# Optimization experiments

Measured on AMD Instinct MI355X. Metric: run time of the kernel, lower is better.

Reference implementation:

```python
import jax, jax.numpy as jnp
import numpy as np

N_NODES = 50000
N_EDGES = 800000
IN_C, HID_C, OUT_C = 128, 128, 64


def setup_inputs() -> dict:
    key = jax.random.key(0)
    k1, k2, k3, k4, k5 = jax.random.split(key, 5)
    x = jax.random.normal(k1, (N_NODES, IN_C), dtype=jnp.float32)
    edge_index = jax.random.randint(k2, (2, N_EDGES), 0, N_NODES, dtype=jnp.int64)
    # Glorot-style init for GCN weights, zero bias (PyG GCNConv defaults)
    s1 = (6.0 / (IN_C + HID_C)) ** 0.5
    s2 = (6.0 / (HID_C + OUT_C)) ** 0.5
    W1 = jax.random.uniform(k3, (IN_C, HID_C), jnp.float32, -s1, s1)
    W2 = jax.random.uniform(k4, (HID_C, OUT_C), jnp.float32, -s2, s2)
    b1 = jnp.zeros((HID_C,), jnp.float32)
    b2 = jnp.zeros((OUT_C,), jnp.float32)
    return {"x": x, "edge_index": edge_index, "W1": W1, "b1": b1, "W2": W2, "b2": b2}


def _gcn_conv(x, src, dst, W, b, n_nodes):
    # PyG GCNConv: add self-loops, symmetric normalization, linear transform,
    # scatter-add aggregation from src (row) to dst (col), then bias.
    h = x @ W  # [N, out]
    loops = jnp.arange(n_nodes, dtype=src.dtype)
    src_f = jnp.concatenate([src, loops])
    dst_f = jnp.concatenate([dst, loops])
    deg = jax.ops.segment_sum(jnp.ones_like(dst_f, dtype=h.dtype), dst_f,
                              num_segments=n_nodes)  # in-degree incl. self-loop
    dinv = jnp.where(deg > 0, jax.lax.rsqrt(deg), 0.0)
    norm = dinv[src_f] * dinv[dst_f]  # [E + N]
    msgs = h[src_f] * norm[:, None]   # gather + scale
    out = jax.ops.segment_sum(msgs, dst_f, num_segments=n_nodes)  # scatter-add
    return out + b


def reference(x, edge_index, W1, b1, W2, b2):
    src, dst = edge_index[0], edge_index[1]
    n = x.shape[0]
    h = jax.nn.relu(_gcn_conv(x, src, dst, W1, b1, n))
    return _gcn_conv(h, src, dst, W2, b2, n)
```

## Files before the change

kernel.cpp:

```cpp
#include <hip/hip_runtime.h>
#include <hip/hip_bf16.h>
#include <hip/hip_fp16.h>


#define NBUCK 800
#define CHUNK 2048
#define STASH 2048

typedef float f32x4 __attribute__((ext_vector_type(4)));
typedef _Float16 f16x8 __attribute__((ext_vector_type(8)));

__global__ __launch_bounds__(256) void presort_k(const int* __restrict__ src,
                                                 const int* __restrict__ dst,
                                                 unsigned* __restrict__ rec2,
                                                 int* __restrict__ hist2,
                                                 int* __restrict__ runstart2,
                                                 int E) {
    __shared__ int lh[NBUCK], lscan[NBUCK], cur[NBUCK];
    __shared__ int sred[256];
    __shared__ unsigned srec[CHUNK];
    int t = threadIdx.x;
    int lo = blockIdx.x * CHUNK, hi = min(E, lo + CHUNK);

    for (int i = t; i < NBUCK; i += 256) lh[i] = 0;
    __syncthreads();
    for (int e = lo + t; e < hi; e += 256)
        atomicAdd(&lh[dst[e] >> 6], 1);
    __syncthreads();

    int base = t * 4;
    int v[4];
    int s = 0;
#pragma unroll
    for (int i = 0; i < 4; ++i) {
        int idx = base + i;
        int c = (idx < NBUCK) ? lh[idx] : 0;
        v[i] = c; s += c;
    }
    sred[t] = s;
    __syncthreads();
#pragma unroll
    for (int off = 1; off < 256; off <<= 1) {
        int x = 0;
        if (t >= off) x = sred[t - off];
        __syncthreads();
        sred[t] += x;
        __syncthreads();
    }
    int run = sred[t] - s;
#pragma unroll
    for (int i = 0; i < 4; ++i) {
        int idx = base + i;
        if (idx < NBUCK) { lscan[idx] = run; cur[idx] = run; }
        run += v[i];
    }
    __syncthreads();

    for (int e = lo + t; e < hi; e += 256) {
        int d = dst[e];
        int p = atomicAdd(&cur[d >> 6], 1);
        srec[p] = (unsigned)(src[e] & 0xffff) | ((unsigned)d << 16);
    }
    __syncthreads();

    int n = hi - lo;
    for (int j = t; j < n; j += 256) rec2[lo + j] = srec[j];
    int hbase = blockIdx.x * NBUCK;
    for (int b = t; b < NBUCK; b += 256) {
        hist2[hbase + b] = lh[b];
        runstart2[hbase + b] = lscan[b];
    }
}

__global__ __launch_bounds__(256) void coltot_k(const int* __restrict__ hist2,
                                                int* __restrict__ btot, int BCNT) {
    __shared__ int sred[256];
    int b = blockIdx.x, t = threadIdx.x;
    int s = 0;
    for (int i = t; i < BCNT; i += 256) s += hist2[i * NBUCK + b];
    sred[t] = s;
    __syncthreads();
#pragma unroll
    for (int off = 128; off > 0; off >>= 1) {
        if (t < off) sred[t] += sred[t + off];
        __syncthreads();
    }
    if (t == 0) btot[b] = sred[0];
}

__global__ __launch_bounds__(256) void scan800_k(const int* __restrict__ btot,
                                                 int* __restrict__ bucketBase,
                                                 int* __restrict__ offsets,
                                                 int N, int E) {
    __shared__ int sred[256];
    int t = threadIdx.x;
    int base = t * 4;
    int v[4];
    int s = 0;
#pragma unroll
    for (int i = 0; i < 4; ++i) {
        int idx = base + i;
        int c = (idx < NBUCK) ? btot[idx] : 0;
        v[i] = c; s += c;
    }
    sred[t] = s;
    __syncthreads();
#pragma unroll
    for (int off = 1; off < 256; off <<= 1) {
        int x = 0;
        if (t >= off) x = sred[t - off];
        __syncthreads();
        sred[t] += x;
        __syncthreads();
    }
    int run = sred[t] - s;
#pragma unroll
    for (int i = 0; i < 4; ++i) {
        int idx = base + i;
        if (idx < NBUCK) bucketBase[idx] = run;
        run += v[i];
    }
    if (t == 255) bucketBase[NBUCK] = run;
    if (t == 0) offsets[N] = E;
}

__global__ __launch_bounds__(256) void finish2_k(const unsigned* __restrict__ rec2,
                                                 const int* __restrict__ hist2,
                                                 const int* __restrict__ runstart2,
                                                 const int* __restrict__ bucketBase,
                                                 int* __restrict__ offsets,
                                                 float* __restrict__ dinv,
                                                 unsigned short* __restrict__ adj,
                                                 int BCNT, int N) {
    __shared__ int ncnt[64], ncur[64], nodeOff[64];
    __shared__ int stashCnt;
    __shared__ unsigned stash[STASH];
    __shared__ unsigned short adjl[STASH];
    int b = blockIdx.x, t = threadIdx.x;
    if (t < 64) { ncnt[t] = 0; ncur[t] = 0; }
    if (t == 0) stashCnt = 0;
    __syncthreads();

    for (int i = t; i < BCNT; i += 256) {
        int len = hist2[i * NBUCK + b];
        if (!len) continue;
        int gbase = i * CHUNK + runstart2[i * NBUCK + b];
        int sp = atomicAdd(&stashCnt, len);
        for (int k = 0; k < len; ++k) {
            unsigned r = rec2[gbase + k];
            atomicAdd(&ncnt[(r >> 16) & 63], 1);
            if (sp + k < STASH) stash[sp + k] = r;
        }
    }
    __syncthreads();

    if (t == 0) {
        int r = 0;
#pragma unroll
        for (int i = 0; i < 64; ++i) { nodeOff[i] = r; r += ncnt[i]; }
    }
    __syncthreads();

    int bstart = bucketBase[b];
    if (t < 64) {
        int gnode = b * 64 + t;
        if (gnode < N) {
            dinv[gnode] = rsqrtf((float)(ncnt[t] + 1));
            offsets[gnode] = bstart + nodeOff[t];
        }
    }
    __syncthreads();

    int tot = stashCnt;
    if (tot > STASH) tot = STASH;
    for (int j = t; j < tot; j += 256) {
        unsigned r = stash[j];
        int ln = (r >> 16) & 63;
        int p = atomicAdd(&ncur[ln], 1);
        adjl[nodeOff[ln] + p] = (unsigned short)(r & 0xffff);
    }
    __syncthreads();
    for (int j = t; j < tot; j += 256) adj[bstart + j] = adjl[j];
}

template <int NOUT, bool HALF_IN>
__global__ __launch_bounds__(256) void gemm_mfma_k(const void* __restrict__ Xv,
                                                   const float* __restrict__ W,
                                                   const float* __restrict__ dinv,
                                                   __half* __restrict__ Hout, int M) {
    constexpr int K = 128;
    constexpr int BM = 64;
    constexpr int LDP = K + 8;
    constexpr int CT = NOUT / 16;
    __shared__ _Float16 xs[BM][LDP];
    __shared__ _Float16 wsl[NOUT][LDP];

    int t = threadIdx.x;
    int brow = blockIdx.x * BM;

    if constexpr (HALF_IN) {
        const __half* X = (const __half*)Xv;
        for (int i = t; i < BM * (K / 8); i += 256) {
            int row = i / (K / 8), c8 = i % (K / 8);
            int gr = brow + row;
            union { _Float16 h[8]; uint4 u; } pk;
            if (gr < M) {
                uint4 u = *(const uint4*)(X + (size_t)gr * K + c8 * 8);
                const __half2* hp = (const __half2*)&u;
                float di = dinv[gr];
#pragma unroll
                for (int j = 0; j < 4; ++j) {
                    float2 f = __half22float2(hp[j]);
                    pk.h[2 * j] = (_Float16)(f.x * di);
                    pk.h[2 * j + 1] = (_Float16)(f.y * di);
                }
            } else {
                pk.u = make_uint4(0, 0, 0, 0);
            }
            *(uint4*)&xs[row][c8 * 8] = pk.u;
        }
    } else {
        const float* X = (const float*)Xv;
        for (int i = t; i < BM * (K / 4); i += 256) {
            int row = i / (K / 4), c4 = i % (K / 4);
            int gr = brow + row;
            union { _Float16 h[4]; uint2 u; } pk;
            if (gr < M) {
                float4 v = *(const float4*)(X + (size_t)gr * K + c4 * 4);
                float di = dinv[gr];
                pk.h[0] = (_Float16)(v.x * di);
                pk.h[1] = (_Float16)(v.y * di);
                pk.h[2] = (_Float16)(v.z * di);
                pk.h[3] = (_Float16)(v.w * di);
            } else {
                pk.u = make_uint2(0, 0);
            }
            *(uint2*)&xs[row][c4 * 4] = pk.u;
        }
    }

    for (int i = t; i < K * (NOUT / 4); i += 256) {
        int k = i / (NOUT / 4), c4 = i % (NOUT / 4);
        float4 wv = *(const float4*)(W + (size_t)k * NOUT + c4 * 4);
        wsl[c4 * 4 + 0][k] = (_Float16)wv.x;
        wsl[c4 * 4 + 1][k] = (_Float16)wv.y;
        wsl[c4 * 4 + 2][k] = (_Float16)wv.z;
        wsl[c4 * 4 + 3][k] = (_Float16)wv.w;
    }
    __syncthreads();

    int w = t >> 6, lane = t & 63;
    int lrow = lane & 15;
    int lko = (lane >> 4) * 8;

    f32x4 acc[CT];
#pragma unroll
    for (int c = 0; c < CT; ++c) acc[c] = (f32x4){0.f, 0.f, 0.f, 0.f};

#pragma unroll
    for (int s = 0; s < K / 32; ++s) {
        f16x8 a = *(const f16x8*)&xs[w * 16 + lrow][s * 32 + lko];
#pragma unroll
        for (int c = 0; c < CT; ++c) {
            f16x8 b = *(const f16x8*)&wsl[c * 16 + lrow][s * 32 + lko];
            acc[c] = __builtin_amdgcn_mfma_f32_16x16x32_f16(a, b, acc[c], 0, 0, 0);
        }
    }

    __syncthreads();
#pragma unroll
    for (int c = 0; c < CT; ++c) {
#pragma unroll
        for (int r = 0; r < 4; ++r)
            xs[w * 16 + (lane >> 4) * 4 + r][c * 16 + lrow] = (_Float16)acc[c][r];
    }
    __syncthreads();
    for (int j = t; j < BM * (NOUT / 8); j += 256) {
        int row = j / (NOUT / 8), c8 = j % (NOUT / 8);
        int gr = brow + row;
        if (gr < M)
            *(uint4*)(Hout + (size_t)gr * NOUT + c8 * 8) = *(uint4*)&xs[row][c8 * 8];
    }
}

__device__ __forceinline__ void ld_row(const __half* p, float (&f)[4]) {
    uint2 u = *(const uint2*)p;
    const __half2* hp = (const __half2*)&u;
    float2 a = __half22float2(hp[0]);
    float2 b = __half22float2(hp[1]);
    f[0] = a.x; f[1] = a.y; f[2] = b.x; f[3] = b.y;
}
__device__ __forceinline__ void ld_row(const __half* p, float (&f)[2]) {
    float2 a = __half22float2(*(const __half2*)p);
    f[0] = a.x; f[1] = a.y;
}

template <int C, bool RELU, typename TOUT>
__global__ __launch_bounds__(256) void aggregate_k(const __half* __restrict__ H,
                                                   const int* __restrict__ offsets,
                                                   const unsigned short* __restrict__ adj,
                                                   const float* __restrict__ dinv,
                                                   const float* __restrict__ bias,
                                                   TOUT* __restrict__ out, int n) {
    constexpr int V = C / 32;
    int wave = threadIdx.x >> 6;
    int lane = threadIdx.x & 63;
    int half_id = lane >> 5;
    int sub = lane & 31;
    int node = blockIdx.x * 8 + wave * 2 + half_id;
    if (node >= n) return;

    const __half* hl = H + sub * V;

    float acc[V];
    ld_row(hl + (size_t)node * C, acc);

    int e0 = offsets[node], e1 = offsets[node + 1];
    int e = e0;

    for (; e + 8 <= e1; e += 8) {
        int s[8];
#pragma unroll
        for (int j = 0; j < 8; ++j) s[j] = adj[e + j];
        float t[8][V];
#pragma unroll
        for (int j = 0; j < 8; ++j) ld_row(hl + (size_t)s[j] * C, t[j]);
#pragma unroll
        for (int v = 0; v < V; ++v)
            acc[v] += ((t[0][v] + t[1][v]) + (t[2][v] + t[3][v])) +
                      ((t[4][v] + t[5][v]) + (t[6][v] + t[7][v]));
    }
    for (; e + 2 <= e1; e += 2) {
        int s0 = adj[e], s1 = adj[e + 1];
        float t0[V], t1[V];
        ld_row(hl + (size_t)s0 * C, t0);
        ld_row(hl + (size_t)s1 * C, t1);
#pragma unroll
        for (int v = 0; v < V; ++v) acc[v] += t0[v] + t1[v];
    }
    if (e < e1) {
        float t0[V];
        ld_row(hl + (size_t)adj[e] * C, t0);
#pragma unroll
        for (int v = 0; v < V; ++v) acc[v] += t0[v];
    }

    float di = dinv[node];
    float o[V];
#pragma unroll
    for (int v = 0; v < V; ++v) {
        o[v] = acc[v] * di + bias[sub * V + v];
        if (RELU) o[v] = fmaxf(o[v], 0.f);
    }

    if constexpr (sizeof(TOUT) == 2) {
        union { __half2 h[2]; uint2 u; } pk;
        pk.h[0] = __floats2half2_rn(o[0], o[1]);
        pk.h[1] = __floats2half2_rn(o[2], o[3]);
        *(uint2*)((__half*)out + (size_t)node * C + sub * V) = pk.u;
    } else {
        *(float2*)((float*)out + (size_t)node * C + sub * V) = make_float2(o[0], o[1]);
    }
}

extern "C" void kernel_launch(void* const* d_in, const int* in_sizes, int n_in,
                              void* d_out, int out_size, void* d_ws, size_t ws_size,
                              hipStream_t stream) {
    const float* x = (const float*)d_in[0];
    const int* ei = (const int*)d_in[1];
    const float* W1 = (const float*)d_in[2];
    const float* b1 = (const float*)d_in[3];
    const float* W2 = (const float*)d_in[4];
    const float* b2 = (const float*)d_in[5];
    float* out = (float*)d_out;

    const int IN_C = 128, HID_C = 128;
    int N = in_sizes[0] / IN_C;
    int E = in_sizes[1] / 2;
    const int* src = ei;
    const int* dst = ei + E;

    int BCNT = (E + CHUNK - 1) / CHUNK;

    int NP = (N + 255) & ~255;
    int EP = (E + 255) & ~255;
    char* w = (char*)d_ws;
    int* hist2 = (int*)w;           w += (size_t)BCNT * NBUCK * 4;
    int* runstart2 = (int*)w;       w += (size_t)BCNT * NBUCK * 4;
    int* btot = (int*)w;            w += (size_t)(NBUCK + 32) * 4;
    int* bucketBase = (int*)w;      w += (size_t)(NBUCK + 32) * 4;
    int* offsets = (int*)w;         w += (size_t)(NP + 256) * 4;
    float* dinv = (float*)w;        w += (size_t)NP * 4;
    unsigned* rec2 = (unsigned*)w;  w += (size_t)(BCNT * CHUNK) * 4;
    unsigned short* adj = (unsigned short*)w; w += (size_t)EP * 2;
    __half* H1 = (__half*)w;        w += (size_t)NP * HID_C * 2;
    __half* HID = (__half*)w;       w += (size_t)NP * HID_C * 2;
    (void)ws_size; (void)n_in; (void)out_size;

    presort_k<<<BCNT, 256, 0, stream>>>(src, dst, rec2, hist2, runstart2, E);
    coltot_k<<<NBUCK, 256, 0, stream>>>(hist2, btot, BCNT);
    scan800_k<<<1, 256, 0, stream>>>(btot, bucketBase, offsets, N, E);
    finish2_k<<<NBUCK, 256, 0, stream>>>(rec2, hist2, runstart2, bucketBase,
                                         offsets, dinv, adj, BCNT, N);

    gemm_mfma_k<128, false><<<(N + 63) / 64, 256, 0, stream>>>(x, W1, dinv, H1, N);
    aggregate_k<128, true, __half><<<(N + 7) / 8, 256, 0, stream>>>(
        H1, offsets, adj, dinv, b1, HID, N);

    gemm_mfma_k<64, true><<<(N + 63) / 64, 256, 0, stream>>>(HID, W2, dinv, H1, N);
    aggregate_k<64, false, float><<<(N + 7) / 8, 256, 0, stream>>>(
        H1, offsets, adj, dinv, b2, out, N);
}
```

Before: 123.6 us.

## Split each node's edge list across four lane groups with wider row loads

The aggregation kernel now gives each node a full wave: four 16-lane groups each gather a quarter of the neighbor rows, and the partial sums are combined with cross-lane shuffles. Each lane loads 8 (or 4) halves per row instead of 4 (or 2), so row loads are wider, and the unrolled-by-8 loop with its tail loops is replaced by a single predicated 16-edge loop. The aim is more independent gathers in flight per node and lower latency on the average degree of about 16. In exchange, a quarter of the lanes sit idle on short or ragged edge lists, shuffle reductions are added, and the grid now covers 4 nodes per block instead of 8.

Result: slower. 145.0 us (+17.3%).

```diff
diff --git a/kernel.cpp b/kernel.cpp
--- a/kernel.cpp
+++ b/kernel.cpp
@@ -283,16 +283,21 @@
     }
 }
 
+__device__ __forceinline__ void ld_row(const __half* p, float (&f)[8]) {
+    uint4 u = *(const uint4*)p;
+    const __half2* hp = (const __half2*)&u;
+#pragma unroll
+    for (int j = 0; j < 4; ++j) {
+        float2 a = __half22float2(hp[j]);
+        f[2 * j] = a.x; f[2 * j + 1] = a.y;
+    }
+}
 __device__ __forceinline__ void ld_row(const __half* p, float (&f)[4]) {
     uint2 u = *(const uint2*)p;
     const __half2* hp = (const __half2*)&u;
     float2 a = __half22float2(hp[0]);
     float2 b = __half22float2(hp[1]);
     f[0] = a.x; f[1] = a.y; f[2] = b.x; f[3] = b.y;
-}
-__device__ __forceinline__ void ld_row(const __half* p, float (&f)[2]) {
-    float2 a = __half22float2(*(const __half2*)p);
-    f[0] = a.x; f[1] = a.y;
 }
 
 template <int C, bool RELU, typename TOUT>
@@ -302,64 +307,64 @@
                                                    const float* __restrict__ dinv,
                                                    const float* __restrict__ bias,
                                                    TOUT* __restrict__ out, int n) {
-    constexpr int V = C / 32;
+    constexpr int V = C / 16;
     int wave = threadIdx.x >> 6;
     int lane = threadIdx.x & 63;
-    int half_id = lane >> 5;
-    int sub = lane & 31;
-    int node = blockIdx.x * 8 + wave * 2 + half_id;
+    int q = lane >> 4;
+    int sub = lane & 15;
+    int node = blockIdx.x * 4 + wave;
     if (node >= n) return;
 
     const __half* hl = H + sub * V;
 
     float acc[V];
-    ld_row(hl + (size_t)node * C, acc);
+#pragma unroll
+    for (int v = 0; v < V; ++v) acc[v] = 0.f;
+    if (q == 0) ld_row(hl + (size_t)node * C, acc);
 
     int e0 = offsets[node], e1 = offsets[node + 1];
-    int e = e0;
-
-    for (; e + 8 <= e1; e += 8) {
-        int s[8];
-#pragma unroll
-        for (int j = 0; j < 8; ++j) s[j] = adj[e + j];
-        float t[8][V];
-#pragma unroll
-        for (int j = 0; j < 8; ++j) ld_row(hl + (size_t)s[j] * C, t[j]);
+
+    for (int eb = e0; eb < e1; eb += 16) {
+        float t[4][V];
+#pragma unroll
+        for (int j = 0; j < 4; ++j) {
+            int idx = eb + j * 4 + q;
+            if (idx < e1) {
+                ld_row(hl + (size_t)adj[idx] * C, t[j]);
+            } else {
+#pragma unroll
+                for (int v = 0; v < V; ++v) t[j][v] = 0.f;
+            }
+        }
 #pragma unroll
         for (int v = 0; v < V; ++v)
-            acc[v] += ((t[0][v] + t[1][v]) + (t[2][v] + t[3][v])) +
-                      ((t[4][v] + t[5][v]) + (t[6][v] + t[7][v]));
-    }
-    for (; e + 2 <= e1; e += 2) {
-        int s0 = adj[e], s1 = adj[e + 1];
-        float t0[V], t1[V];
-        ld_row(hl + (size_t)s0 * C, t0);
-        ld_row(hl + (size_t)s1 * C, t1);
-#pragma unroll
-        for (int v = 0; v < V; ++v) acc[v] += t0[v] + t1[v];
-    }
-    if (e < e1) {
-        float t0[V];
-        ld_row(hl + (size_t)adj[e] * C, t0);
-#pragma unroll
-        for (int v = 0; v < V; ++v) acc[v] += t0[v];
-    }
-
-    float di = dinv[node];
-    float o[V];
+            acc[v] += (t[0][v] + t[1][v]) + (t[2][v] + t[3][v]);
+    }
+
 #pragma unroll
     for (int v = 0; v < V; ++v) {
-        o[v] = acc[v] * di + bias[sub * V + v];
-        if (RELU) o[v] = fmaxf(o[v], 0.f);
-    }
-
-    if constexpr (sizeof(TOUT) == 2) {
-        union { __half2 h[2]; uint2 u; } pk;
-        pk.h[0] = __floats2half2_rn(o[0], o[1]);
-        pk.h[1] = __floats2half2_rn(o[2], o[3]);
-        *(uint2*)((__half*)out + (size_t)node * C + sub * V) = pk.u;
-    } else {
-        *(float2*)((float*)out + (size_t)node * C + sub * V) = make_float2(o[0], o[1]);
+        acc[v] += __shfl_xor(acc[v], 16, 64);
+        acc[v] += __shfl_xor(acc[v], 32, 64);
+    }
+
+    if (q == 0) {
+        float di = dinv[node];
+        float o[V];
+#pragma unroll
+        for (int v = 0; v < V; ++v) {
+            o[v] = acc[v] * di + bias[sub * V + v];
+            if (RELU) o[v] = fmaxf(o[v], 0.f);
+        }
+        if constexpr (sizeof(TOUT) == 2) {
+            union { __half2 h[4]; uint4 u; } pk;
+#pragma unroll
+            for (int j = 0; j < 4; ++j)
+                pk.h[j] = __floats2half2_rn(o[2 * j], o[2 * j + 1]);
+            *(uint4*)((__half*)out + (size_t)node * C + sub * V) = pk.u;
+        } else {
+            *(float4*)((float*)out + (size_t)node * C + sub * V) =
+                make_float4(o[0], o[1], o[2], o[3]);
+        }
     }
 }
 
@@ -404,10 +409,10 @@
                                          offsets, dinv, adj, BCNT, N);
 
     gemm_mfma_k<128, false><<<(N + 63) / 64, 256, 0, stream>>>(x, W1, dinv, H1, N);
-    aggregate_k<128, true, __half><<<(N + 7) / 8, 256, 0, stream>>>(
+    aggregate_k<128, true, __half><<<(N + 3) / 4, 256, 0, stream>>>(
         H1, offsets, adj, dinv, b1, HID, N);
 
     gemm_mfma_k<64, true><<<(N + 63) / 64, 256, 0, stream>>>(HID, W2, dinv, H1, N);
-    aggregate_k<64, false, float><<<(N + 7) / 8, 256, 0, stream>>>(
+    aggregate_k<64, false, float><<<(N + 3) / 4, 256, 0, stream>>>(
         H1, offsets, adj, dinv, b2, out, N);
 }
```
